# Optimization experiments

Hardware: AMD Instinct MI355X
Metric: run time of the kernel (lower is better)

Reference implementation:

```python
import jax, jax.numpy as jnp
import numpy as np

B, N, C, L = 16, 50176, 256, 16

def setup_inputs() -> dict:
    key = jax.random.key(0)
    k1, k2 = jax.random.split(key)
    X = jax.random.normal(k1, (B, N, C), dtype=jnp.float32)
    # xavier_uniform over fan_in=256, fan_out=L=16
    bound = float(np.sqrt(6.0 / (C + L)))
    Wa = jax.random.uniform(k2, (B, C, L), dtype=jnp.float32, minval=-bound, maxval=bound)
    return {"X": X, "Wa": Wa}

def reference(X, Wa):
    # A: [B, N, L] attention scores per token slot
    A = jnp.einsum('bnc,bcl->bnl', X, Wa)
    A = jax.nn.softmax(A, axis=1)          # softmax over the N tokens
    # T: [B, L, C] pooled tokens = A^T @ X
    return jnp.einsum('bnl,bnc->blc', A, X)
```

## Files before the change

### kernel.cpp

```cpp
#include <hip/hip_runtime.h>


#define BATCH 16
#define NTOK  50176
#define CH    256
#define LDIM  16
#define CHUNK 64
#define GPB   48
#define NCHUNK (NTOK / CHUNK)

typedef __bf16 bf16x8 __attribute__((ext_vector_type(8)));
typedef float  f32x4  __attribute__((ext_vector_type(4)));

#define XS_STRIDE 264
#define WT_STRIDE 264
#define WK_STRIDE 72

template <bool USE_PARTIALS>
__global__ __launch_bounds__(256, 3)
void tok_main(const float* __restrict__ X, const float* __restrict__ Wa,
              float* __restrict__ Tout, float* __restrict__ sout)
{
    __shared__ __align__(16) __bf16 Xs[CHUNK][XS_STRIDE];
    __shared__ __align__(16) __bf16 Wt[LDIM][WT_STRIDE];
    __shared__ __align__(16) __bf16 wT[LDIM][WK_STRIDE];
    __shared__ float s_lds[LDIM];

    const int tid  = threadIdx.x;
    const int wave = tid >> 6;
    const int lane = tid & 63;
    const int quad = lane >> 4;
    const int l16  = lane & 15;

    const int b = blockIdx.x / GPB;
    const int g = blockIdx.x % GPB;

    {
        const float* wrow = Wa + ((size_t)b * CH + tid) * LDIM;
        #pragma unroll
        for (int l = 0; l < LDIM; ++l)
            Wt[l][tid] = (__bf16)wrow[l];
    }
    if (tid < LDIM) s_lds[tid] = 0.0f;

    f32x4 acc[4];
    #pragma unroll
    for (int t = 0; t < 4; ++t) acc[t] = (f32x4){0.f, 0.f, 0.f, 0.f};
    float s_acc[4] = {0.f, 0.f, 0.f, 0.f};

    const float* Xb = X + (size_t)b * NTOK * CH;

    for (int chunk = g; chunk < NCHUNK; chunk += GPB) {
        const float* Xc = Xb + (size_t)chunk * CHUNK * CH;
        __syncthreads();
        #pragma unroll
        for (int j = 0; j < 16; ++j) {
            const int f   = j * 256 + tid;
            const int tok = f >> 6;
            const int c4  = (f & 63) << 2;
            const float4 v = *(const float4*)(Xc + tok * CH + c4);
            __bf16* dst = &Xs[tok][c4];
            dst[0] = (__bf16)v.x; dst[1] = (__bf16)v.y;
            dst[2] = (__bf16)v.z; dst[3] = (__bf16)v.w;
        }
        __syncthreads();

        f32x4 d = (f32x4){0.f, 0.f, 0.f, 0.f};
        #pragma unroll
        for (int ks = 0; ks < 8; ++ks) {
            const bf16x8 a  = *(const bf16x8*)&Wt[l16][ks * 32 + quad * 8];
            const bf16x8 bb = *(const bf16x8*)&Xs[wave * 16 + l16][ks * 32 + quad * 8];
            d = __builtin_amdgcn_mfma_f32_16x16x32_bf16(a, bb, d, 0, 0, 0);
        }
        #pragma unroll
        for (int r = 0; r < 4; ++r) {
            const float e = __expf(d[r]);
            s_acc[r] += e;
            wT[quad * 4 + r][wave * 16 + l16] = (__bf16)e;
        }
        __syncthreads();

        #pragma unroll
        for (int ks = 0; ks < 2; ++ks) {
            const bf16x8 a = *(const bf16x8*)&wT[l16][ks * 32 + quad * 8];
            #pragma unroll
            for (int t = 0; t < 4; ++t) {
                const int c = (wave * 4 + t) * 16 + l16;
                bf16x8 bb;
                #pragma unroll
                for (int j = 0; j < 8; ++j)
                    bb[j] = Xs[ks * 32 + quad * 8 + j][c];
                acc[t] = __builtin_amdgcn_mfma_f32_16x16x32_bf16(a, bb, acc[t], 0, 0, 0);
            }
        }
    }

    #pragma unroll
    for (int r = 0; r < 4; ++r)
        atomicAdd(&s_lds[quad * 4 + r], s_acc[r]);
    __syncthreads();

    if (USE_PARTIALS) {
        if (tid < LDIM)
            sout[((size_t)b * GPB + g) * LDIM + tid] = s_lds[tid];
        float* Tb = Tout + ((size_t)b * GPB + g) * LDIM * CH;
        #pragma unroll
        for (int t = 0; t < 4; ++t) {
            const int c = (wave * 4 + t) * 16 + l16;
            #pragma unroll
            for (int r = 0; r < 4; ++r)
                Tb[(quad * 4 + r) * CH + c] = acc[t][r];
        }
    } else {
        if (tid < LDIM) atomicAdd(&sout[b * LDIM + tid], s_lds[tid]);
        float* Tb = Tout + (size_t)b * LDIM * CH;
        #pragma unroll
        for (int t = 0; t < 4; ++t) {
            const int c = (wave * 4 + t) * 16 + l16;
            #pragma unroll
            for (int r = 0; r < 4; ++r)
                atomicAdd(&Tb[(quad * 4 + r) * CH + c], acc[t][r]);
        }
    }
}

__global__ void tok_reduce_part(const float* __restrict__ Tp, const float* __restrict__ sp,
                                float* __restrict__ out)
{
    const int bl = blockIdx.x;
    const int c  = threadIdx.x;
    const int b = bl >> 4, l = bl & 15;
    float sum = 0.f, st = 0.f;
    for (int g = 0; g < GPB; ++g) {
        sum += Tp[(((size_t)b * GPB + g) * LDIM + l) * CH + c];
        st  += sp[((size_t)b * GPB + g) * LDIM + l];
    }
    out[(size_t)bl * CH + c] = sum / st;
}

__global__ void tok_reduce_atomic(const float* __restrict__ Tacc, const float* __restrict__ sacc,
                                  float* __restrict__ out)
{
    const int bl = blockIdx.x;
    const int c  = threadIdx.x;
    out[(size_t)bl * CH + c] = Tacc[(size_t)bl * CH + c] / sacc[bl];
}

extern "C" void kernel_launch(void* const* d_in, const int* in_sizes, int n_in,
                              void* d_out, int out_size, void* d_ws, size_t ws_size,
                              hipStream_t stream)
{
    const float* X  = (const float*)d_in[0];
    const float* Wa = (const float*)d_in[1];
    float* out = (float*)d_out;

    const size_t part_elems = (size_t)BATCH * GPB * LDIM * CH;
    const size_t sp_elems   = (size_t)BATCH * GPB * LDIM;
    const size_t need_part  = (part_elems + sp_elems) * sizeof(float);

    if (ws_size >= need_part) {
        float* Tp = (float*)d_ws;
        float* sp = Tp + part_elems;
        tok_main<true><<<BATCH * GPB, 256, 0, stream>>>(X, Wa, Tp, sp);
        tok_reduce_part<<<BATCH * LDIM, CH, 0, stream>>>(Tp, sp, out);
    } else {
        float* Tacc = (float*)d_ws;
        float* sacc = Tacc + (size_t)BATCH * LDIM * CH;
        hipMemsetAsync(d_ws, 0,
                       ((size_t)BATCH * LDIM * CH + BATCH * LDIM) * sizeof(float), stream);
        tok_main<false><<<BATCH * GPB, 256, 0, stream>>>(X, Wa, Tacc, sacc);
        tok_reduce_atomic<<<BATCH * LDIM, CH, 0, stream>>>(Tacc, sacc, out);
    }
}
```

Baseline: 1.036 ms.

## Register-prefetch next X chunk and hoist Wa fragments into registers

Loads of the next chunk's X are issued into a 16-entry float4 register buffer right after the LDS store, so global memory latency overlaps with the two MFMA phases. Each wave's 16 global loads now cover 16 rows per instruction, and the bf16 stores to LDS are 4-wide vectors instead of scalars. The Wa operand fragments are loaded from LDS once, before the loop, instead of on every chunk. This adds about 64 VGPRs for the buffer plus 32 for the weights, which may lower occupancy under the 3-blocks launch bound or cause spills.

```diff
diff --git a/kernel.cpp b/kernel.cpp
--- a/kernel.cpp
+++ b/kernel.cpp
@@ -10,10 +10,10 @@
 #define NCHUNK (NTOK / CHUNK)
 
 typedef __bf16 bf16x8 __attribute__((ext_vector_type(8)));
+typedef __bf16 bf16x4 __attribute__((ext_vector_type(4)));
 typedef float  f32x4  __attribute__((ext_vector_type(4)));
 
 #define XS_STRIDE 264
-#define WT_STRIDE 264
 #define WK_STRIDE 72
 
 template <bool USE_PARTIALS>
@@ -22,7 +22,7 @@
               float* __restrict__ Tout, float* __restrict__ sout)
 {
     __shared__ __align__(16) __bf16 Xs[CHUNK][XS_STRIDE];
-    __shared__ __align__(16) __bf16 Wt[LDIM][WT_STRIDE];
+    __shared__ __align__(16) __bf16 Wt[LDIM][CH + 8];
     __shared__ __align__(16) __bf16 wT[LDIM][WK_STRIDE];
     __shared__ float s_lds[LDIM];
 
@@ -42,6 +42,12 @@
             Wt[l][tid] = (__bf16)wrow[l];
     }
     if (tid < LDIM) s_lds[tid] = 0.0f;
+    __syncthreads();
+
+    bf16x8 a_w[8];
+    #pragma unroll
+    for (int ks = 0; ks < 8; ++ks)
+        a_w[ks] = *(const bf16x8*)&Wt[l16][ks * 32 + quad * 8];
 
     f32x4 acc[4];
     #pragma unroll
@@ -50,27 +56,39 @@
 
     const float* Xb = X + (size_t)b * NTOK * CH;
 
-    for (int chunk = g; chunk < NCHUNK; chunk += GPB) {
-        const float* Xc = Xb + (size_t)chunk * CHUNK * CH;
+    f32x4 buf[16];
+    int chunk = g;
+    {
+        const float* Xc = Xb + (size_t)chunk * CHUNK * CH + wave * CH + lane * 4;
+        #pragma unroll
+        for (int j = 0; j < 16; ++j)
+            buf[j] = *(const f32x4*)(Xc + (size_t)j * 4 * CH);
+    }
+
+    while (chunk < NCHUNK) {
         __syncthreads();
         #pragma unroll
         for (int j = 0; j < 16; ++j) {
-            const int f   = j * 256 + tid;
-            const int tok = f >> 6;
-            const int c4  = (f & 63) << 2;
-            const float4 v = *(const float4*)(Xc + tok * CH + c4);
-            __bf16* dst = &Xs[tok][c4];
-            dst[0] = (__bf16)v.x; dst[1] = (__bf16)v.y;
-            dst[2] = (__bf16)v.z; dst[3] = (__bf16)v.w;
+            bf16x4 o;
+            o[0] = (__bf16)buf[j][0]; o[1] = (__bf16)buf[j][1];
+            o[2] = (__bf16)buf[j][2]; o[3] = (__bf16)buf[j][3];
+            *(bf16x4*)&Xs[j * 4 + wave][lane * 4] = o;
         }
         __syncthreads();
+
+        const int next = chunk + GPB;
+        if (next < NCHUNK) {
+            const float* Xc = Xb + (size_t)next * CHUNK * CH + wave * CH + lane * 4;
+            #pragma unroll
+            for (int j = 0; j < 16; ++j)
+                buf[j] = *(const f32x4*)(Xc + (size_t)j * 4 * CH);
+        }
 
         f32x4 d = (f32x4){0.f, 0.f, 0.f, 0.f};
         #pragma unroll
         for (int ks = 0; ks < 8; ++ks) {
-            const bf16x8 a  = *(const bf16x8*)&Wt[l16][ks * 32 + quad * 8];
             const bf16x8 bb = *(const bf16x8*)&Xs[wave * 16 + l16][ks * 32 + quad * 8];
-            d = __builtin_amdgcn_mfma_f32_16x16x32_bf16(a, bb, d, 0, 0, 0);
+            d = __builtin_amdgcn_mfma_f32_16x16x32_bf16(a_w[ks], bb, d, 0, 0, 0);
         }
         #pragma unroll
         for (int r = 0; r < 4; ++r) {
@@ -93,6 +111,7 @@
                 acc[t] = __builtin_amdgcn_mfma_f32_16x16x32_bf16(a, bb, acc[t], 0, 0, 0);
             }
         }
+        chunk = next;
     }
 
     #pragma unroll
```

New measurement: 1.023 ms. No clear change (-1.2%).
